# Performance work log

Hardware: AMD Instinct MI355X
Metric: run time of the kernel (lower is better)

Reference implementation:

```python
import jax, jax.numpy as jnp
import numpy as np

B, C, K = 256, 512, 5  # k_size=5 from g_channels=512, gamma=2, b=1

def _conv1d(x, w):
    # x: (B, 1, C), w: (1, 1, K), 'same' padding, no bias
    pad = (K - 1) // 2
    return jax.lax.conv_general_dilated(
        x, w, window_strides=(1,), padding=[(pad, pad)],
        dimension_numbers=("NCH", "OIH", "NCH"))

def setup_inputs() -> dict:
    key = jax.random.key(0)
    kq, kk, kv, kwq, kwk, kwv = jax.random.split(key, 6)
    return {
        "q": jax.random.normal(kq, (B, 1, C), dtype=jnp.float32),
        "k": jax.random.normal(kk, (B, 1, C), dtype=jnp.float32),
        "v": jax.random.normal(kv, (B, 1, C), dtype=jnp.float32),
        "wq": jax.random.normal(kwq, (1, 1, K), dtype=jnp.float32) * 0.3,
        "wk": jax.random.normal(kwk, (1, 1, K), dtype=jnp.float32) * 0.3,
        "wv": jax.random.normal(kwv, (1, 1, K), dtype=jnp.float32) * 0.3,
    }

def reference(q, k, v, wq, wk, wv):
    # conv then transpose(-1,-2): (B,1,C) -> (B,C,1)
    qh = jnp.transpose(_conv1d(q, wq), (0, 2, 1))  # (B, C, 1)
    kh = jnp.transpose(_conv1d(k, wk), (0, 2, 1))  # (B, C, 1)
    vh = jnp.transpose(_conv1d(v, wv), (0, 2, 1))  # (B, C, 1)
    scale = jnp.sqrt(jnp.float32(qh.shape[-1]))    # sqrt(1) = 1, kept for fidelity
    scores = jnp.einsum("bci,bdi->bcd", qh, kh) / scale  # (B, C, C)
    attn = jax.nn.softmax(scores, axis=-1)
    weighted = jnp.einsum("bcd,bdi->bci", attn, vh)      # (B, C, 1)
    return weighted[..., None, None]  # (B, C, 1, 1, 1)
```

## Files before the change

### kernel.cpp

```cpp
#include <hip/hip_runtime.h>

constexpr int BATCH = 256;
constexpr int CH    = 512;
constexpr int KS    = 5;
constexpr int PAD   = (KS - 1) / 2;

__global__ __launch_bounds__(CH, 2) void attn1d_kernel(
    const float* __restrict__ q, const float* __restrict__ k, const float* __restrict__ v,
    const float* __restrict__ wq, const float* __restrict__ wk, const float* __restrict__ wv,
    float* __restrict__ out)
{
    __shared__ float sq[CH], sk[CH], sv[CH];
    __shared__ float kh[CH], vh[CH];
    __shared__ float wred_max[8], wred_min[8];
    __shared__ float s_kmax, s_kmin;

    const int b = blockIdx.x;
    const int t = threadIdx.x;

    sq[t] = q[b * CH + t];
    sk[t] = k[b * CH + t];
    sv[t] = v[b * CH + t];

    float w_q[KS], w_k[KS], w_v[KS];
#pragma unroll
    for (int j = 0; j < KS; ++j) { w_q[j] = wq[j]; w_k[j] = wk[j]; w_v[j] = wv[j]; }
    __syncthreads();

    float aq = 0.f, ak = 0.f, av = 0.f;
#pragma unroll
    for (int j = 0; j < KS; ++j) {
        const int idx = t + j - PAD;
        if (idx >= 0 && idx < CH) {
            aq = fmaf(sq[idx], w_q[j], aq);
            ak = fmaf(sk[idx], w_k[j], ak);
            av = fmaf(sv[idx], w_v[j], av);
        }
    }
    kh[t] = ak;
    vh[t] = av;

    float lmax = ak, lmin = ak;
#pragma unroll
    for (int off = 32; off > 0; off >>= 1) {
        lmax = fmaxf(lmax, __shfl_down(lmax, off, 64));
        lmin = fminf(lmin, __shfl_down(lmin, off, 64));
    }
    const int wave = t >> 6;
    if ((t & 63) == 0) { wred_max[wave] = lmax; wred_min[wave] = lmin; }
    __syncthreads();
    if (t == 0) {
        float m = wred_max[0], n = wred_min[0];
#pragma unroll
        for (int i = 1; i < 8; ++i) { m = fmaxf(m, wred_max[i]); n = fminf(n, wred_min[i]); }
        s_kmax = m; s_kmin = n;
    }
    __syncthreads();

    const float qc = aq;
    const float m = (qc >= 0.f) ? qc * s_kmax : qc * s_kmin;

    float den = 0.f, num = 0.f;
    const float4* kh4 = (const float4*)kh;
    const float4* vh4 = (const float4*)vh;
#pragma unroll 4
    for (int d4 = 0; d4 < CH / 4; ++d4) {
        const float4 kk = kh4[d4];
        const float4 vv = vh4[d4];
        const float e0 = __expf(fmaf(qc, kk.x, -m));
        const float e1 = __expf(fmaf(qc, kk.y, -m));
        const float e2 = __expf(fmaf(qc, kk.z, -m));
        const float e3 = __expf(fmaf(qc, kk.w, -m));
        den += (e0 + e1) + (e2 + e3);
        num = fmaf(e0, vv.x, num);
        num = fmaf(e1, vv.y, num);
        num = fmaf(e2, vv.z, num);
        num = fmaf(e3, vv.w, num);
    }

    out[b * CH + t] = num / den;
}

extern "C" void kernel_launch(void* const* d_in, const int* in_sizes, int n_in,
                              void* d_out, int out_size, void* d_ws, size_t ws_size,
                              hipStream_t stream) {
    const float* q  = (const float*)d_in[0];
    const float* k  = (const float*)d_in[1];
    const float* v  = (const float*)d_in[2];
    const float* wq = (const float*)d_in[3];
    const float* wk = (const float*)d_in[4];
    const float* wv = (const float*)d_in[5];
    float* out = (float*)d_out;

    attn1d_kernel<<<BATCH, CH, 0, stream>>>(q, k, v, wq, wk, wv, out);
}
```

Baseline: 74.48 us.

## Split conv and attention into two kernels, halving key range per thread

```diff
diff --git a/kernel.cpp b/kernel.cpp
--- a/kernel.cpp
+++ b/kernel.cpp
@@ -4,16 +4,16 @@
 constexpr int CH    = 512;
 constexpr int KS    = 5;
 constexpr int PAD   = (KS - 1) / 2;
+constexpr float LOG2E = 1.4426950408889634f;
 
-__global__ __launch_bounds__(CH, 2) void attn1d_kernel(
+
+__global__ __launch_bounds__(CH, 2) void conv_stats_kernel(
     const float* __restrict__ q, const float* __restrict__ k, const float* __restrict__ v,
     const float* __restrict__ wq, const float* __restrict__ wk, const float* __restrict__ wv,
-    float* __restrict__ out)
+    float* __restrict__ ws)
 {
     __shared__ float sq[CH], sk[CH], sv[CH];
-    __shared__ float kh[CH], vh[CH];
     __shared__ float wred_max[8], wred_min[8];
-    __shared__ float s_kmax, s_kmin;
 
     const int b = blockIdx.x;
     const int t = threadIdx.x;
@@ -37,8 +37,10 @@
             av = fmaf(sv[idx], w_v[j], av);
         }
     }
-    kh[t] = ak;
-    vh[t] = av;
+
+    ws[b * CH + t]                 = aq * LOG2E;
+    ws[(BATCH + b) * CH + t]       = ak;
+    ws[(2 * BATCH + b) * CH + t]   = av;
 
     float lmax = ak, lmin = ak;
 #pragma unroll
@@ -53,32 +55,55 @@
         float m = wred_max[0], n = wred_min[0];
 #pragma unroll
         for (int i = 1; i < 8; ++i) { m = fmaxf(m, wred_max[i]); n = fminf(n, wred_min[i]); }
-        s_kmax = m; s_kmin = n;
+        float* kstat = ws + 3 * BATCH * CH;
+        kstat[2 * b]     = m;
+        kstat[2 * b + 1] = n;
     }
+}
+
+__global__ __launch_bounds__(1024, 4) void attn1d_kernel(
+    const float* __restrict__ qh2g, const float* __restrict__ khg,
+    const float* __restrict__ vhg,  const float* __restrict__ kstat,
+    float* __restrict__ out)
+{
+    __shared__ float redd[CH], redn[CH];
+
+    const int b = blockIdx.x;
+    const int t = threadIdx.x;
+    const int c = t & (CH - 1);
+    const int h = __builtin_amdgcn_readfirstlane(t >> 9);
+
+    const float qc2 = qh2g[b * CH + c];
+    const float kmax = kstat[2 * b];
+    const float kmin = kstat[2 * b + 1];
+    const float m2  = (qc2 >= 0.f) ? qc2 * kmax : qc2 * kmin;
+    const float nm2 = -m2;
+
+    const float4* __restrict__ k4 = (const float4*)(khg + b * CH + h * (CH / 2));
+    const float4* __restrict__ v4 = (const float4*)(vhg + b * CH + h * (CH / 2));
+
+    float den0 = 0.f, den1 = 0.f, den2 = 0.f, den3 = 0.f;
+    float num0 = 0.f, num1 = 0.f, num2 = 0.f, num3 = 0.f;
+#pragma unroll 4
+    for (int i = 0; i < (CH / 2) / 4; ++i) {
+        const float4 kk = k4[i];
+        const float4 vv = v4[i];
+        const float e0 = __builtin_amdgcn_exp2f(fmaf(qc2, kk.x, nm2));
+        const float e1 = __builtin_amdgcn_exp2f(fmaf(qc2, kk.y, nm2));
+        const float e2 = __builtin_amdgcn_exp2f(fmaf(qc2, kk.z, nm2));
+        const float e3 = __builtin_amdgcn_exp2f(fmaf(qc2, kk.w, nm2));
+        den0 += e0; den1 += e1; den2 += e2; den3 += e3;
+        num0 = fmaf(e0, vv.x, num0);
+        num1 = fmaf(e1, vv.y, num1);
+        num2 = fmaf(e2, vv.z, num2);
+        num3 = fmaf(e3, vv.w, num3);
+    }
+    const float den = (den0 + den1) + (den2 + den3);
+    const float num = (num0 + num1) + (num2 + num3);
+
+    if (h == 1) { redd[c] = den; redn[c] = num; }
     __syncthreads();
-
-    const float qc = aq;
-    const float m = (qc >= 0.f) ? qc * s_kmax : qc * s_kmin;
-
-    float den = 0.f, num = 0.f;
-    const float4* kh4 = (const float4*)kh;
-    const float4* vh4 = (const float4*)vh;
-#pragma unroll 4
-    for (int d4 = 0; d4 < CH / 4; ++d4) {
-        const float4 kk = kh4[d4];
-        const float4 vv = vh4[d4];
-        const float e0 = __expf(fmaf(qc, kk.x, -m));
-        const float e1 = __expf(fmaf(qc, kk.y, -m));
-        const float e2 = __expf(fmaf(qc, kk.z, -m));
-        const float e3 = __expf(fmaf(qc, kk.w, -m));
-        den += (e0 + e1) + (e2 + e3);
-        num = fmaf(e0, vv.x, num);
-        num = fmaf(e1, vv.y, num);
-        num = fmaf(e2, vv.z, num);
-        num = fmaf(e3, vv.w, num);
-    }
-
-    out[b * CH + t] = num / den;
+    if (h == 0) out[b * CH + c] = (num + redn[c]) / (den + redd[c]);
 }
 
 extern "C" void kernel_launch(void* const* d_in, const int* in_sizes, int n_in,
@@ -91,6 +116,13 @@
     const float* wk = (const float*)d_in[4];
     const float* wv = (const float*)d_in[5];
     float* out = (float*)d_out;
+    float* ws  = (float*)d_ws;
 
-    attn1d_kernel<<<BATCH, CH, 0, stream>>>(q, k, v, wq, wk, wv, out);
+    conv_stats_kernel<<<BATCH, CH, 0, stream>>>(q, k, v, wq, wk, wv, ws);
+
+    const float* qh2g  = ws;
+    const float* khg   = ws + BATCH * CH;
+    const float* vhg   = ws + 2 * BATCH * CH;
+    const float* kstat = ws + 3 * BATCH * CH;
+    attn1d_kernel<<<BATCH, 1024, 0, stream>>>(qh2g, khg, vhg, kstat, out);
 }
```

Result: no change. 75.20 us (+1.0%).

## Split key dimension across thread groups with register-blocked query rows and exp2

Applied to the files above, without the earlier changes.

```diff
diff --git a/kernel.cpp b/kernel.cpp
--- a/kernel.cpp
+++ b/kernel.cpp
@@ -4,50 +4,56 @@
 constexpr int CH    = 512;
 constexpr int KS    = 5;
 constexpr int PAD   = (KS - 1) / 2;
+constexpr float LOG2E = 1.4426950408889634f;
 
-__global__ __launch_bounds__(CH, 2) void attn1d_kernel(
+__global__ __launch_bounds__(1024, 1) void fused_attn1d_kernel(
     const float* __restrict__ q, const float* __restrict__ k, const float* __restrict__ v,
     const float* __restrict__ wq, const float* __restrict__ wk, const float* __restrict__ wv,
     float* __restrict__ out)
 {
-    __shared__ float sq[CH], sk[CH], sv[CH];
-    __shared__ float kh[CH], vh[CH];
+    __shared__ __align__(16) float sq[CH], sk[CH], sv[CH];
+    __shared__ __align__(16) float qh2[CH], kh[CH], vh[CH];
+    __shared__ float2 red[8][CH];
     __shared__ float wred_max[8], wred_min[8];
     __shared__ float s_kmax, s_kmin;
 
     const int b = blockIdx.x;
     const int t = threadIdx.x;
 
-    sq[t] = q[b * CH + t];
-    sk[t] = k[b * CH + t];
-    sv[t] = v[b * CH + t];
-
-    float w_q[KS], w_k[KS], w_v[KS];
-#pragma unroll
-    for (int j = 0; j < KS; ++j) { w_q[j] = wq[j]; w_k[j] = wk[j]; w_v[j] = wv[j]; }
+    if (t < CH) {
+        sq[t] = q[b * CH + t];
+        sk[t] = k[b * CH + t];
+        sv[t] = v[b * CH + t];
+    }
     __syncthreads();
 
-    float aq = 0.f, ak = 0.f, av = 0.f;
+    if (t < CH) {
+        float w_q[KS], w_k[KS], w_v[KS];
 #pragma unroll
-    for (int j = 0; j < KS; ++j) {
-        const int idx = t + j - PAD;
-        if (idx >= 0 && idx < CH) {
-            aq = fmaf(sq[idx], w_q[j], aq);
-            ak = fmaf(sk[idx], w_k[j], ak);
-            av = fmaf(sv[idx], w_v[j], av);
+        for (int j = 0; j < KS; ++j) { w_q[j] = wq[j]; w_k[j] = wk[j]; w_v[j] = wv[j]; }
+
+        float aq = 0.f, ak = 0.f, av = 0.f;
+#pragma unroll
+        for (int j = 0; j < KS; ++j) {
+            const int idx = t + j - PAD;
+            if (idx >= 0 && idx < CH) {
+                aq = fmaf(sq[idx], w_q[j], aq);
+                ak = fmaf(sk[idx], w_k[j], ak);
+                av = fmaf(sv[idx], w_v[j], av);
+            }
         }
+        qh2[t] = aq * LOG2E;
+        kh[t]  = ak;
+        vh[t]  = av;
+
+        float lmax = ak, lmin = ak;
+#pragma unroll
+        for (int off = 32; off > 0; off >>= 1) {
+            lmax = fmaxf(lmax, __shfl_down(lmax, off, 64));
+            lmin = fminf(lmin, __shfl_down(lmin, off, 64));
+        }
+        if ((t & 63) == 0) { wred_max[t >> 6] = lmax; wred_min[t >> 6] = lmin; }
     }
-    kh[t] = ak;
-    vh[t] = av;
-
-    float lmax = ak, lmin = ak;
-#pragma unroll
-    for (int off = 32; off > 0; off >>= 1) {
-        lmax = fmaxf(lmax, __shfl_down(lmax, off, 64));
-        lmin = fminf(lmin, __shfl_down(lmin, off, 64));
-    }
-    const int wave = t >> 6;
-    if ((t & 63) == 0) { wred_max[wave] = lmax; wred_min[wave] = lmin; }
     __syncthreads();
     if (t == 0) {
         float m = wred_max[0], n = wred_min[0];
@@ -57,28 +63,52 @@
     }
     __syncthreads();
 
-    const float qc = aq;
-    const float m = (qc >= 0.f) ? qc * s_kmax : qc * s_kmin;
+    const int g  = t >> 7;
+    const int li = t & 127;
 
-    float den = 0.f, num = 0.f;
+    float qr[4], nm2[4];
+    float den[4] = {0.f, 0.f, 0.f, 0.f};
+    float num[4] = {0.f, 0.f, 0.f, 0.f};
+#pragma unroll
+    for (int r = 0; r < 4; ++r) {
+        const float qc2 = qh2[li + 128 * r];
+        qr[r]  = qc2;
+        nm2[r] = -((qc2 >= 0.f) ? qc2 * s_kmax : qc2 * s_kmin);
+    }
+
     const float4* kh4 = (const float4*)kh;
     const float4* vh4 = (const float4*)vh;
+    const int base = g * 16;
 #pragma unroll 4
-    for (int d4 = 0; d4 < CH / 4; ++d4) {
-        const float4 kk = kh4[d4];
-        const float4 vv = vh4[d4];
-        const float e0 = __expf(fmaf(qc, kk.x, -m));
-        const float e1 = __expf(fmaf(qc, kk.y, -m));
-        const float e2 = __expf(fmaf(qc, kk.z, -m));
-        const float e3 = __expf(fmaf(qc, kk.w, -m));
-        den += (e0 + e1) + (e2 + e3);
-        num = fmaf(e0, vv.x, num);
-        num = fmaf(e1, vv.y, num);
-        num = fmaf(e2, vv.z, num);
-        num = fmaf(e3, vv.w, num);
+    for (int i = 0; i < 16; ++i) {
+        const float4 kk = kh4[base + i];
+        const float4 vv = vh4[base + i];
+#pragma unroll
+        for (int r = 0; r < 4; ++r) {
+            const float e0 = __builtin_amdgcn_exp2f(fmaf(qr[r], kk.x, nm2[r]));
+            const float e1 = __builtin_amdgcn_exp2f(fmaf(qr[r], kk.y, nm2[r]));
+            const float e2 = __builtin_amdgcn_exp2f(fmaf(qr[r], kk.z, nm2[r]));
+            const float e3 = __builtin_amdgcn_exp2f(fmaf(qr[r], kk.w, nm2[r]));
+            den[r] += (e0 + e1) + (e2 + e3);
+            num[r] = fmaf(e0, vv.x, num[r]);
+            num[r] = fmaf(e1, vv.y, num[r]);
+            num[r] = fmaf(e2, vv.z, num[r]);
+            num[r] = fmaf(e3, vv.w, num[r]);
+        }
     }
+#pragma unroll
+    for (int r = 0; r < 4; ++r) red[g][li + 128 * r] = make_float2(num[r], den[r]);
+    __syncthreads();
 
-    out[b * CH + t] = num / den;
+    if (t < CH) {
+        float n = 0.f, d = 0.f;
+#pragma unroll
+        for (int g2 = 0; g2 < 8; ++g2) {
+            const float2 p = red[g2][t];
+            n += p.x; d += p.y;
+        }
+        out[b * CH + t] = n / d;
+    }
 }
 
 extern "C" void kernel_launch(void* const* d_in, const int* in_sizes, int n_in,
@@ -91,6 +121,7 @@
     const float* wk = (const float*)d_in[4];
     const float* wv = (const float*)d_in[5];
     float* out = (float*)d_out;
+    (void)d_ws; (void)ws_size;
 
-    attn1d_kernel<<<BATCH, CH, 0, stream>>>(q, k, v, wq, wk, wv, out);
+    fused_attn1d_kernel<<<BATCH, 1024, 0, stream>>>(q, k, v, wq, wk, wv, out);
 }
```

After: 72.98 us. -2.0%, faster.
